# Kernel tuning notes

Hardware: AMD Instinct MI355X
Metric: run time of the kernel (lower is better)

The kernel has to match this reference:

```python
import jax, jax.numpy as jnp
import numpy as np

T, B, E = 512, 128, 256  # timesteps, batch_size, embedding_size


def setup_inputs() -> dict:
    key = jax.random.key(0)
    k1, k2, k3 = jax.random.split(key, 3)
    return {
        "v": jax.random.normal(k1, (T, B, E), dtype=jnp.float32),
        "u": jax.random.uniform(k2, (T, B), dtype=jnp.float32),  # pop signals in (0,1)
        "d": jax.random.uniform(k3, (T, B), dtype=jnp.float32),  # push signals in (0,1)
    }


def _pop(s, w):
    """Grefenstette-stack pop: s [T,B] strengths (stack grows along dim 0,
    padded with zeros past the current depth), w [B] pop amount.
    Reverse cumsum, subtract w, clamp at 0, then difference to recover per-slot
    strengths. Zero padding at the tail is preserved exactly (contributes 0)."""
    top = jnp.cumsum(s[::-1], axis=0) - w[None, :]
    top = jnp.clip(top, 0.0)
    top = top - jnp.concatenate([jnp.zeros_like(top[:1]), top[:-1]], axis=0)
    return top[::-1]


def reference(v, u, d):
    # v: [T, B, E] pushed vectors; u, d: [T, B] pop/push strengths.
    T_, B_ = u.shape
    E_ = v.shape[-1]
    ones = jnp.ones((B_,), v.dtype)

    def step(carry, xs):
        V, s = carry  # V: [T,B,E] value buffer, s: [T,B] strengths (zero-padded)
        t, v_t, u_t, d_t = xs
        V = V.at[t].set(v_t)
        # forward(): pop with u (original detaches s and u inside pop), then push d
        s = _pop(jax.lax.stop_gradient(s), jax.lax.stop_gradient(u_t)).at[t].set(d_t)
        # read(): weights = s - pop(s, 1); r = sum_t weights * V
        weights = s - _pop(jax.lax.stop_gradient(s), ones)
        r = jnp.einsum('tb,tbe->be', weights, V)
        return (V, s), r

    init = (jnp.zeros((T_, B_, E_), v.dtype), jnp.zeros((T_, B_), v.dtype))
    _, rs = jax.lax.scan(step, init, (jnp.arange(T_), v, u, d))
    return rs  # [T, B, E] read vector at each timestep
```

## Files before the change

### kernel.cpp

```cpp
#include <hip/hip_runtime.h>

#define T_DIM 512
#define B_DIM 128
#define E_DIM 256
#define NEG_INF (-1e30f)


struct Node { float g; int ngl; };

__global__ void __launch_bounds__(512) scan_prep(
    const float* __restrict__ u, const float* __restrict__ d,
    float* __restrict__ S_out, Node* __restrict__ nodes)
{
    const int b    = blockIdx.x;
    const int t    = threadIdx.x;
    const int lane = t & 63;
    const int w    = t >> 6;

    __shared__ float wsum[8];
    __shared__ float wpre[8];
    __shared__ float M[10][T_DIM];

    const float dv = d[t * B_DIM + b];
    float x = dv - u[t * B_DIM + b];

    #pragma unroll
    for (int off = 1; off < 64; off <<= 1) {
        float y = __shfl_up(x, off, 64);
        if (lane >= off) x += y;
    }
    if (lane == 63) wsum[w] = x;
    __syncthreads();
    if (t < 8) {
        float s = 0.f;
        for (int i = 0; i < t; ++i) s += wsum[i];
        wpre[t] = s;
    }
    __syncthreads();
    const float S = x + wpre[w];
    const float g = dv - S;

    M[0][t] = g;
    __syncthreads();
    #pragma unroll
    for (int k = 1; k < 10; ++k) {
        int h = 1 << (k - 1);
        float left = (t >= h) ? M[k - 1][t - h] : NEG_INF;
        float mk = fmaxf(M[k - 1][t], left);
        __syncthreads();
        M[k][t] = mk;
        __syncthreads();
    }

    int m = t - 1;
    #pragma unroll
    for (int k = 9; k >= 0; --k) {
        if (m >= 0 && M[k][m] <= g) m -= (1 << k);
    }
    if (m < 0) m = -1;

    S_out[(b << 9) | t] = S;
    nodes[(b << 9) | t] = Node{g, m};
}

__global__ void __launch_bounds__(256) stack_read(
    const float* __restrict__ v, const float* __restrict__ S_in,
    const Node* __restrict__ nodes, float* __restrict__ out)
{
    const int wid  = (blockIdx.x << 2) | (threadIdx.x >> 6);
    const int lane = threadIdx.x & 63;
    const int id0  = wid << 1, id1 = id0 | 1;
    const int b0 = id0 >> 9, t0 = id0 & 511;
    const int b1 = id1 >> 9, t1 = id1 & 511;
    const int e4 = lane << 2;

    const float S0 = S_in[id0];
    const float S1 = S_in[id1];
    const Node* __restrict__ nb0 = nodes + (b0 << 9);
    const Node* __restrict__ nb1 = nodes + (b1 << 9);

    float4 acc0 = {0.f,0.f,0.f,0.f}, acc1 = {0.f,0.f,0.f,0.f};
    float prev0 = 0.f, prev1 = 0.f;
    int m0 = t0, m1 = t1;
    bool act0 = true, act1 = true;

    while (act0 || act1) {
        Node nd0, nd1; float4 vv0, vv1;
        if (act0) {
            nd0 = nb0[m0];
            vv0 = *(const float4*)(v + ((size_t)m0 * B_DIM + b0) * E_DIM + e4);
        }
        if (act1) {
            nd1 = nb1[m1];
            vv1 = *(const float4*)(v + ((size_t)m1 * B_DIM + b1) * E_DIM + e4);
        }
        if (act0) {
            float rc = S0 + nd0.g;
            float cur = fminf(rc, 1.f);
            float wt = cur - prev0;
            acc0.x += wt * vv0.x; acc0.y += wt * vv0.y;
            acc0.z += wt * vv0.z; acc0.w += wt * vv0.w;
            prev0 = cur;
            if (rc >= 1.f || nd0.ngl < 0) act0 = false; else m0 = nd0.ngl;
        }
        if (act1) {
            float rc = S1 + nd1.g;
            float cur = fminf(rc, 1.f);
            float wt = cur - prev1;
            acc1.x += wt * vv1.x; acc1.y += wt * vv1.y;
            acc1.z += wt * vv1.z; acc1.w += wt * vv1.w;
            prev1 = cur;
            if (rc >= 1.f || nd1.ngl < 0) act1 = false; else m1 = nd1.ngl;
        }
    }
    *(float4*)(out + ((size_t)t0 * B_DIM + b0) * E_DIM + e4) = acc0;
    *(float4*)(out + ((size_t)t1 * B_DIM + b1) * E_DIM + e4) = acc1;
}

extern "C" void kernel_launch(void* const* d_in, const int* in_sizes, int n_in,
                              void* d_out, int out_size, void* d_ws, size_t ws_size,
                              hipStream_t stream) {
    const float* v = (const float*)d_in[0];
    const float* u = (const float*)d_in[1];
    const float* d = (const float*)d_in[2];
    float* out = (float*)d_out;

    float* S    = (float*)d_ws;
    Node*  node = (Node*)((char*)d_ws + (size_t)B_DIM * T_DIM * 4);

    scan_prep<<<dim3(B_DIM), 512, 0, stream>>>(u, d, S, node);
    stack_read<<<dim3((T_DIM * B_DIM) / 8), 256, 0, stream>>>(v, S, node, out);
}
```

Before: 138.1 us.

## Precompute per-slot stack-read chains in prep kernel to batch gather loads

The prep kernel now walks each timestep's next-greater-left chain in shared memory, up to 16 entries. It stores the (weight, index) pairs in a staged LDS buffer, copies them to a global list, and writes tail state to an aux array. The read kernel then uses one wave per (b,t). It broadcasts the precomputed indices with shuffles and issues four independent v gathers per iteration instead of chasing dependent node loads. Chains longer than 16 fall back to the original pointer walk. The cost is a much heavier prep kernel (serial per-thread walk, 64KB of LDS staging, an extra ~8MB list write and read) and half as much per-wave work in the read kernel.

```diff
diff --git a/kernel.cpp b/kernel.cpp
--- a/kernel.cpp
+++ b/kernel.cpp
@@ -3,6 +3,7 @@
 #define T_DIM 512
 #define B_DIM 128
 #define E_DIM 256
+#define L_CAP 16
 #define NEG_INF (-1e30f)
 
 
@@ -10,7 +11,7 @@
 
 __global__ void __launch_bounds__(512) scan_prep(
     const float* __restrict__ u, const float* __restrict__ d,
-    float* __restrict__ S_out, Node* __restrict__ nodes)
+    Node* __restrict__ nodes, float2* __restrict__ lists, int4* __restrict__ aux)
 {
     const int b    = blockIdx.x;
     const int t    = threadIdx.x;
@@ -20,6 +21,8 @@
     __shared__ float wsum[8];
     __shared__ float wpre[8];
     __shared__ float M[10][T_DIM];
+    __shared__ int   ngl_s[T_DIM];
+    __shared__ float2 stage[T_DIM * L_CAP];
 
     const float dv = d[t * B_DIM + b];
     float x = dv - u[t * B_DIM + b];
@@ -58,63 +61,97 @@
         if (m >= 0 && M[k][m] <= g) m -= (1 << k);
     }
     if (m < 0) m = -1;
+    ngl_s[t] = m;
+    nodes[(b << 9) | t] = Node{g, m};
+    __syncthreads();
 
-    S_out[(b << 9) | t] = S;
-    nodes[(b << 9) | t] = Node{g, m};
+    float2* mystage = &stage[t * L_CAP];
+    float prev = 0.f;
+    int mcur = t, cnt = 0, tailm = -1;
+    float tailprev = 0.f;
+    #pragma unroll 1
+    for (;;) {
+        float gm = M[0][mcur];
+        float rc = S + gm;
+        float cur = fminf(rc, 1.f);
+        mystage[cnt] = make_float2(cur - prev, __int_as_float(mcur));
+        ++cnt; prev = cur;
+        int nx = ngl_s[mcur];
+        if (rc >= 1.f || nx < 0) break;
+        if (cnt == L_CAP) { tailm = nx; tailprev = prev; break; }
+        mcur = nx;
+    }
+    aux[(b << 9) | t] = make_int4(cnt, tailm, __float_as_int(tailprev), __float_as_int(S));
+    __syncthreads();
+
+    float4* gl = (float4*)(lists + (size_t)(b << 9) * L_CAP);
+    const float4* st = (const float4*)stage;
+    #pragma unroll
+    for (int i = 0; i < (T_DIM * L_CAP) / 2 / 512; ++i)
+        gl[i * 512 + t] = st[i * 512 + t];
 }
 
 __global__ void __launch_bounds__(256) stack_read(
-    const float* __restrict__ v, const float* __restrict__ S_in,
-    const Node* __restrict__ nodes, float* __restrict__ out)
+    const float* __restrict__ v, const Node* __restrict__ nodes,
+    const float2* __restrict__ lists, const int4* __restrict__ aux,
+    float* __restrict__ out)
 {
     const int wid  = (blockIdx.x << 2) | (threadIdx.x >> 6);
     const int lane = threadIdx.x & 63;
-    const int id0  = wid << 1, id1 = id0 | 1;
-    const int b0 = id0 >> 9, t0 = id0 & 511;
-    const int b1 = id1 >> 9, t1 = id1 & 511;
+    const int b = wid >> 9;
+    const int t = wid & 511;
     const int e4 = lane << 2;
+    const float* __restrict__ vb = v + (size_t)b * E_DIM + e4;
 
-    const float S0 = S_in[id0];
-    const float S1 = S_in[id1];
-    const Node* __restrict__ nb0 = nodes + (b0 << 9);
-    const Node* __restrict__ nb1 = nodes + (b1 << 9);
+    const int4 ax = aux[wid];
+    const int cnt = ax.x;
 
-    float4 acc0 = {0.f,0.f,0.f,0.f}, acc1 = {0.f,0.f,0.f,0.f};
-    float prev0 = 0.f, prev1 = 0.f;
-    int m0 = t0, m1 = t1;
-    bool act0 = true, act1 = true;
+    float2 pr = lists[(size_t)wid * L_CAP + (lane & 15)];
+    float my_w = pr.x;
+    int   my_m = __float_as_int(pr.y);
 
-    while (act0 || act1) {
-        Node nd0, nd1; float4 vv0, vv1;
-        if (act0) {
-            nd0 = nb0[m0];
-            vv0 = *(const float4*)(v + ((size_t)m0 * B_DIM + b0) * E_DIM + e4);
+    float4 acc = {0.f, 0.f, 0.f, 0.f};
+    const int nc = (cnt + 3) >> 2;
+    #pragma unroll 1
+    for (int c = 0; c < nc; ++c) {
+        float wj[4]; float4 vj[4];
+        #pragma unroll
+        for (int j = 0; j < 4; ++j) {
+            int idx = (c << 2) + j;
+            int   mj = __shfl(my_m, idx, 64);
+            float ww = __shfl(my_w, idx, 64);
+            bool on = idx < cnt;
+            mj = on ? mj : t;
+            wj[j] = on ? ww : 0.f;
+            vj[j] = *(const float4*)(vb + (size_t)mj * (B_DIM * E_DIM));
         }
-        if (act1) {
-            nd1 = nb1[m1];
-            vv1 = *(const float4*)(v + ((size_t)m1 * B_DIM + b1) * E_DIM + e4);
-        }
-        if (act0) {
-            float rc = S0 + nd0.g;
-            float cur = fminf(rc, 1.f);
-            float wt = cur - prev0;
-            acc0.x += wt * vv0.x; acc0.y += wt * vv0.y;
-            acc0.z += wt * vv0.z; acc0.w += wt * vv0.w;
-            prev0 = cur;
-            if (rc >= 1.f || nd0.ngl < 0) act0 = false; else m0 = nd0.ngl;
-        }
-        if (act1) {
-            float rc = S1 + nd1.g;
-            float cur = fminf(rc, 1.f);
-            float wt = cur - prev1;
-            acc1.x += wt * vv1.x; acc1.y += wt * vv1.y;
-            acc1.z += wt * vv1.z; acc1.w += wt * vv1.w;
-            prev1 = cur;
-            if (rc >= 1.f || nd1.ngl < 0) act1 = false; else m1 = nd1.ngl;
+        #pragma unroll
+        for (int j = 0; j < 4; ++j) {
+            acc.x += wj[j] * vj[j].x; acc.y += wj[j] * vj[j].y;
+            acc.z += wj[j] * vj[j].z; acc.w += wj[j] * vj[j].w;
         }
     }
-    *(float4*)(out + ((size_t)t0 * B_DIM + b0) * E_DIM + e4) = acc0;
-    *(float4*)(out + ((size_t)t1 * B_DIM + b1) * E_DIM + e4) = acc1;
+
+    if (ax.y >= 0) {
+        const float S = __int_as_float(ax.w);
+        float prev = __int_as_float(ax.z);
+        int m = ax.y;
+        const Node* __restrict__ nb = nodes + (b << 9);
+        while (true) {
+            Node nd = nb[m];
+            float rc = S + nd.g;
+            float cur = fminf(rc, 1.f);
+            float ww = cur - prev;
+            float4 vv = *(const float4*)(vb + (size_t)m * (B_DIM * E_DIM));
+            acc.x += ww * vv.x; acc.y += ww * vv.y;
+            acc.z += ww * vv.z; acc.w += ww * vv.w;
+            prev = cur;
+            if (rc >= 1.f || nd.ngl < 0) break;
+            m = nd.ngl;
+        }
+    }
+
+    *(float4*)(out + ((size_t)t * B_DIM + b) * E_DIM + e4) = acc;
 }
 
 extern "C" void kernel_launch(void* const* d_in, const int* in_sizes, int n_in,
@@ -125,9 +162,11 @@
     const float* d = (const float*)d_in[2];
     float* out = (float*)d_out;
 
-    float* S    = (float*)d_ws;
-    Node*  node = (Node*)((char*)d_ws + (size_t)B_DIM * T_DIM * 4);
+    char* ws = (char*)d_ws;
+    Node*   node = (Node*)ws;
+    float2* list = (float2*)(ws + (1 << 19));
+    int4*   aux  = (int4*)(ws + (1 << 19) + (1 << 23));
 
-    scan_prep<<<dim3(B_DIM), 512, 0, stream>>>(u, d, S, node);
-    stack_read<<<dim3((T_DIM * B_DIM) / 8), 256, 0, stream>>>(v, S, node, out);
+    scan_prep<<<dim3(B_DIM), 512, 0, stream>>>(u, d, node, list, aux);
+    stack_read<<<dim3((T_DIM * B_DIM) / 4), 256, 0, stream>>>(v, node, list, aux, out);
 }
```

After: 139.7 us. No clear change (+1.1%).
